# Kernel tuning notes

Hardware: AMD Instinct MI355X
Metric: run time of the kernel (lower is better)

Reference implementation:

```python
import jax, jax.numpy as jnp
import numpy as np


def setup_inputs() -> dict:
    key = jax.random.key(0)
    ks = jax.random.split(key, 5)
    B, N, Fin, Fout = 8, 2048, 512, 512
    stdv = 1.0 / np.sqrt(Fout)
    w_stdv = 1.0 / np.sqrt(Fin)
    x = jax.random.normal(ks[0], (B, N, Fin), dtype=jnp.float32)
    weight = jax.random.uniform(ks[1], (Fin, Fout), dtype=jnp.float32, minval=-stdv, maxval=stdv)
    bias = jax.random.uniform(ks[2], (Fout,), dtype=jnp.float32, minval=-stdv, maxval=stdv)
    w_one = jax.random.uniform(ks[3], (Fin, Fin), dtype=jnp.float32, minval=-w_stdv, maxval=w_stdv)
    w_two = jax.random.uniform(ks[4], (Fin, Fin), dtype=jnp.float32, minval=-w_stdv, maxval=w_stdv)
    return {"x": x, "weight": weight, "bias": bias, "w_one": w_one, "w_two": w_two}


def reference(x, weight, bias, w_one, w_two):
    # x: [B, N, Fin]
    support = jnp.einsum('bnf,fo->bno', x, weight)          # [B, N, Fout]
    phi_one = jnp.einsum('ef,bnf->ben', w_one, x)           # [B, Fin, N]
    phi_two = jnp.einsum('ef,bnf->ben', w_two, x)           # [B, Fin, N]
    adj = jnp.einsum('ben,bem->bnm', phi_one, phi_two)      # [B, N, N]
    adj = jax.nn.softmax(adj, axis=1)                        # softmax over dim=1 (columns)
    out = jnp.einsum('bnm,bmo->bno', adj, support)           # [B, N, Fout]
    return out + bias
```

## Files before the change

### kernel.cpp

```cpp
#include <hip/hip_runtime.h>
#include <math.h>

#define BB 8
#define NN 2048
#define FF 512

typedef __attribute__((ext_vector_type(8))) short short8;
typedef __attribute__((ext_vector_type(4))) float floatx4;

__device__ __forceinline__ unsigned short f2bf(float f) {
    union { float f; unsigned u; } v; v.f = f;
    unsigned r = v.u + 0x7FFFu + ((v.u >> 16) & 1u);
    return (unsigned short)(r >> 16);
}

__global__ __launch_bounds__(256) void gemm_mfma_bt(
    const unsigned short* __restrict__ A, const unsigned short* __restrict__ B,
    void* __restrict__ Cv, const float* __restrict__ bias, float* __restrict__ Dsum,
    int M, int Nc, int K, int a_ld, int b_ld, int ldc,
    long a_batch, long b_batch, long c_batch, int mode)
{
    __shared__ __align__(16) unsigned short Alds[128 * 64];
    __shared__ __align__(16) unsigned short Blds[128 * 64];

    const int tid  = threadIdx.x;
    const int wave = tid >> 6;
    const int lane = tid & 63;
    const int bz   = blockIdx.z;

    const unsigned short* Ab = A + (long)bz * a_batch;
    const unsigned short* Bb = B + (long)bz * b_batch;

    const int m0 = blockIdx.y * 128;
    const int n0 = blockIdx.x * 128;

    const int wm   = (wave >> 1) * 64;
    const int wn   = (wave & 1) * 64;
    const int fl   = lane & 15;
    const int quad = lane >> 4;

    floatx4 acc[4][4] = {};

    for (int k0 = 0; k0 < K; k0 += 64) {
        #pragma unroll
        for (int issue = 0; issue < 4; ++issue) {
            const int cbase = issue * 256 + wave * 64;
            const int c = cbase + lane;
            const int row = c >> 3;
            const int kq = ((c & 7) ^ ((c >> 3) & 7)) * 8;
            const unsigned short* gA = Ab + (long)(m0 + row) * a_ld + k0 + kq;
            __builtin_amdgcn_global_load_lds(
                (const __attribute__((address_space(1))) void*)gA,
                (__attribute__((address_space(3))) void*)&Alds[cbase * 8], 16, 0, 0);
            const unsigned short* gB = Bb + (long)(n0 + row) * b_ld + k0 + kq;
            __builtin_amdgcn_global_load_lds(
                (const __attribute__((address_space(1))) void*)gB,
                (__attribute__((address_space(3))) void*)&Blds[cbase * 8], 16, 0, 0);
        }
        __syncthreads();

        #pragma unroll
        for (int s = 0; s < 2; ++s) {
            short8 af[4], bf[4];
            #pragma unroll
            for (int i = 0; i < 4; ++i) {
                const int slot = ((s * 4 + quad) ^ (fl & 7)) * 8;
                af[i] = *(const short8*)&Alds[(wm + i * 16 + fl) * 64 + slot];
            }
            #pragma unroll
            for (int j = 0; j < 4; ++j) {
                const int slot = ((s * 4 + quad) ^ (fl & 7)) * 8;
                bf[j] = *(const short8*)&Blds[(wn + j * 16 + fl) * 64 + slot];
            }
            #pragma unroll
            for (int i = 0; i < 4; ++i)
                #pragma unroll
                for (int j = 0; j < 4; ++j)
                    acc[i][j] = __builtin_amdgcn_mfma_f32_16x16x32_bf16(af[i], bf[j], acc[i][j], 0, 0, 0);
        }
        __syncthreads();
    }

    if (mode == 0) {
        float* Cb = (float*)Cv + (long)bz * c_batch;
        #pragma unroll
        for (int j = 0; j < 4; ++j) {
            const int ng = n0 + wn + j * 16 + fl;
            const float badd = bias ? bias[ng] : 0.0f;
            #pragma unroll
            for (int i = 0; i < 4; ++i) {
                const int mg = m0 + wm + i * 16 + quad * 4;
                #pragma unroll
                for (int r = 0; r < 4; ++r)
                    Cb[(long)(mg + r) * ldc + ng] = acc[i][j][r] + badd;
            }
        }
    } else if (mode == 1) {
        unsigned short* Cb = (unsigned short*)Cv + (long)bz * c_batch;
        #pragma unroll
        for (int j = 0; j < 4; ++j) {
            const int ng = n0 + wn + j * 16 + fl;
            #pragma unroll
            for (int i = 0; i < 4; ++i) {
                const int mg = m0 + wm + i * 16 + quad * 4;
                #pragma unroll
                for (int r = 0; r < 4; ++r)
                    Cb[(long)(mg + r) * ldc + ng] = f2bf(acc[i][j][r]);
            }
        }
    } else {
        unsigned short* Cb = (unsigned short*)Cv + (long)bz * c_batch;
        float* Db = Dsum + (long)bz * NN;
        #pragma unroll
        for (int j = 0; j < 4; ++j) {
            const int ng = n0 + wn + j * 16 + fl;
            float csum = 0.f;
            #pragma unroll
            for (int i = 0; i < 4; ++i) {
                const int mg = m0 + wm + i * 16 + quad * 4;
                #pragma unroll
                for (int r = 0; r < 4; ++r) {
                    const float e = __expf(acc[i][j][r]);
                    csum += e;
                    Cb[(long)(mg + r) * ldc + ng] = f2bf(e);
                }
            }
            csum += __shfl_xor(csum, 16);
            csum += __shfl_xor(csum, 32);
            if (quad == 0) atomicAdd(&Db[ng], csum);
        }
    }
}

__global__ __launch_bounds__(256) void convert_all(
    const float* __restrict__ x, const float* __restrict__ w1, const float* __restrict__ w2,
    unsigned short* __restrict__ xb, unsigned short* __restrict__ w1b, unsigned short* __restrict__ w2b)
{
    const long NX = (long)BB * NN * FF / 8;
    const long NW = (long)FF * FF / 8;
    long t = (long)blockIdx.x * 256 + threadIdx.x;
    const float* in; unsigned short* out;
    if (t < NX) { in = x; out = xb; }
    else if (t < NX + NW) { in = w1; out = w1b; t -= NX; }
    else if (t < NX + 2 * NW) { in = w2; out = w2b; t -= NX + NW; }
    else return;
    const long i = t * 8;
    float4 a = *(const float4*)(in + i);
    float4 b = *(const float4*)(in + i + 4);
    short8 o;
    o[0] = (short)f2bf(a.x); o[1] = (short)f2bf(a.y);
    o[2] = (short)f2bf(a.z); o[3] = (short)f2bf(a.w);
    o[4] = (short)f2bf(b.x); o[5] = (short)f2bf(b.y);
    o[6] = (short)f2bf(b.z); o[7] = (short)f2bf(b.w);
    *(short8*)(out + i) = o;
}

__global__ __launch_bounds__(256) void transpose_convert(
    const float* __restrict__ in, unsigned short* __restrict__ out, int dim)
{
    __shared__ float t[32][33];
    const int tx = threadIdx.x & 31, ty = threadIdx.x >> 5;
    const int x0 = blockIdx.x * 32, y0 = blockIdx.y * 32;
    #pragma unroll
    for (int k = 0; k < 32; k += 8)
        t[ty + k][tx] = in[(long)(y0 + ty + k) * dim + x0 + tx];
    __syncthreads();
    #pragma unroll
    for (int k = 0; k < 32; k += 8)
        out[(long)(x0 + ty + k) * dim + y0 + tx] = f2bf(t[tx][ty + k]);
}

__global__ __launch_bounds__(256) void zero_f32(float* __restrict__ p, long n)
{
    long i = (long)blockIdx.x * 256 + threadIdx.x;
    if (i < n) p[i] = 0.0f;
}

__global__ __launch_bounds__(256) void scale_transpose(
    const unsigned short* __restrict__ Call, const float* __restrict__ D,
    unsigned short* __restrict__ supT, int batch0)
{
    __shared__ float t[32][33];
    __shared__ float rD[32];
    const int tx = threadIdx.x & 31, ty = threadIdx.x >> 5;
    const int mt = blockIdx.x * 32, ot = blockIdx.y * 32;
    const int b = batch0 + blockIdx.z;
    const unsigned short* Cb = Call + (long)b * NN * 1536;
    unsigned short* Tb = supT + (long)b * NN * FF;
    if (threadIdx.x < 32) rD[threadIdx.x] = 1.0f / D[(long)b * NN + mt + threadIdx.x];
    __syncthreads();
    #pragma unroll
    for (int k = 0; k < 32; k += 8) {
        unsigned short u = Cb[(long)(mt + ty + k) * 1536 + 1024 + ot + tx];
        union { unsigned uu; float f; } cv; cv.uu = ((unsigned)u) << 16;
        t[ty + k][tx] = cv.f;
    }
    __syncthreads();
    #pragma unroll
    for (int k = 0; k < 32; k += 8)
        Tb[(long)(ot + ty + k) * NN + mt + tx] = f2bf(t[tx][ty + k] * rD[tx]);
}

extern "C" void kernel_launch(void* const* d_in, const int* in_sizes, int n_in,
                              void* d_out, int out_size, void* d_ws, size_t ws_size,
                              hipStream_t stream)
{
    const float* x      = (const float*)d_in[0];
    const float* weight = (const float*)d_in[1];
    const float* bias   = (const float*)d_in[2];
    const float* w_one  = (const float*)d_in[3];
    const float* w_two  = (const float*)d_in[4];
    float* out = (float*)d_out;

    const long NF  = (long)NN * FF;
    const long NN2 = (long)NN * NN;
    const long CROW = 1536;

    char* p = (char*)d_ws;
    unsigned short* xb    = (unsigned short*)p; p += (size_t)BB * NF * 2;
    unsigned short* Wall  = (unsigned short*)p; p += (size_t)CROW * FF * 2;
    unsigned short* Call  = (unsigned short*)p; p += (size_t)BB * NN * CROW * 2;
    unsigned short* supT  = (unsigned short*)p; p += (size_t)BB * NF * 2;
    float*          Dsum  = (float*)p;          p += (size_t)BB * NN * 4;
    unsigned short* E     = (unsigned short*)p;
    unsigned short* w1b = Wall;
    unsigned short* w2b = Wall + (size_t)FF * FF;
    unsigned short* wTb = Wall + (size_t)2 * FF * FF;

    const size_t fixed = (size_t)(p - (char*)d_ws);
    const bool full = ws_size >= fixed + (size_t)BB * NN2 * 2;

    dim3 blk(256);

    convert_all<<<dim3(4352), blk, 0, stream>>>(x, w_one, w_two, xb, w1b, w2b);
    transpose_convert<<<dim3(FF / 32, FF / 32), blk, 0, stream>>>(weight, wTb, FF);
    zero_f32<<<dim3((BB * NN) / 256), blk, 0, stream>>>(Dsum, BB * NN);

    gemm_mfma_bt<<<dim3(CROW / 128, NN / 128, BB), blk, 0, stream>>>(
        xb, Wall, Call, nullptr, nullptr, NN, (int)CROW, FF,
        FF, FF, (int)CROW, NF, 0, NN * CROW, 1);

    if (full) {
        gemm_mfma_bt<<<dim3(NN / 128, NN / 128, BB), blk, 0, stream>>>(
            Call, Call + FF, E, nullptr, Dsum, NN, NN, FF,
            (int)CROW, (int)CROW, NN, NN * CROW, NN * CROW, NN2, 2);
        scale_transpose<<<dim3(NN / 32, FF / 32, BB), blk, 0, stream>>>(Call, Dsum, supT, 0);
        gemm_mfma_bt<<<dim3(FF / 128, NN / 128, BB), blk, 0, stream>>>(
            E, supT, out, bias, nullptr, NN, FF, NN,
            NN, NN, FF, NN2, NF, NF, 0);
    } else {
        for (int b = 0; b < BB; ++b) {
            const unsigned short* Cb = Call + (size_t)b * NN * CROW;
            gemm_mfma_bt<<<dim3(NN / 128, NN / 128, 1), blk, 0, stream>>>(
                Cb, Cb + FF, E, nullptr, Dsum + (size_t)b * NN, NN, NN, FF,
                (int)CROW, (int)CROW, NN, 0, 0, 0, 2);
            scale_transpose<<<dim3(NN / 32, FF / 32, 1), blk, 0, stream>>>(Call, Dsum, supT, b);
            gemm_mfma_bt<<<dim3(FF / 128, NN / 128, 1), blk, 0, stream>>>(
                E, supT + (size_t)b * NF, out + (size_t)b * NF, bias, nullptr, NN, FF, NN,
                NN, NN, FF, 0, 0, 0, 0);
        }
    }
}
```

Baseline: 240.7 us.

## Fold log2e into w_one, use exp2, packed bf16 converts, hoist GEMM addressing

Scales w_one by log2(e) during the bf16 conversion so the softmax epilogue can call a native exp2 in place of __expf. Replaces the software bf16 rounding with packed hardware conversions in the epilogues and the convert kernel. Hoists the per-thread global-load offsets out of the K loop and advances the base pointers instead. Pre-scaling before bf16 rounding slightly changes the rounding of w_one, and the epilogue stores are still scalar 16-bit writes.

```diff
diff --git a/kernel.cpp b/kernel.cpp
--- a/kernel.cpp
+++ b/kernel.cpp
@@ -4,14 +4,33 @@
 #define BB 8
 #define NN 2048
 #define FF 512
+#define LOG2E 1.4426950408889634f
 
 typedef __attribute__((ext_vector_type(8))) short short8;
 typedef __attribute__((ext_vector_type(4))) float floatx4;
+typedef __attribute__((ext_vector_type(2))) float float2v;
+typedef __attribute__((ext_vector_type(2))) __bf16 bf16x2;
 
 __device__ __forceinline__ unsigned short f2bf(float f) {
     union { float f; unsigned u; } v; v.f = f;
     unsigned r = v.u + 0x7FFFu + ((v.u >> 16) & 1u);
     return (unsigned short)(r >> 16);
+}
+
+__device__ __forceinline__ float fexp2(float x) {
+#if __has_builtin(__builtin_amdgcn_exp2f)
+    return __builtin_amdgcn_exp2f(x);
+#else
+    return __expf(x * 0.69314718056f);
+#endif
+}
+
+__device__ __forceinline__ void pk_store(unsigned short* p0, unsigned short* p1,
+                                         float a, float b) {
+    union { bf16x2 h; unsigned short s[2]; } u;
+    float2v v; v.x = a; v.y = b;
+    u.h = __builtin_convertvector(v, bf16x2);
+    *p0 = u.s[0]; *p1 = u.s[1];
 }
 
 __global__ __launch_bounds__(256) void gemm_mfma_bt(
@@ -28,50 +47,54 @@
     const int lane = tid & 63;
     const int bz   = blockIdx.z;
 
-    const unsigned short* Ab = A + (long)bz * a_batch;
-    const unsigned short* Bb = B + (long)bz * b_batch;
-
     const int m0 = blockIdx.y * 128;
     const int n0 = blockIdx.x * 128;
+
+    const unsigned short* Aptr = A + (long)bz * a_batch + (long)m0 * a_ld;
+    const unsigned short* Bptr = B + (long)bz * b_batch + (long)n0 * b_ld;
 
     const int wm   = (wave >> 1) * 64;
     const int wn   = (wave & 1) * 64;
     const int fl   = lane & 15;
     const int quad = lane >> 4;
 
+    int offA[4], offB[4], cb[4];
+    #pragma unroll
+    for (int issue = 0; issue < 4; ++issue) {
+        const int cbase = issue * 256 + wave * 64;
+        const int c = cbase + lane;
+        const int row = c >> 3;
+        const int kq = ((c & 7) ^ ((c >> 3) & 7)) * 8;
+        offA[issue] = row * a_ld + kq;
+        offB[issue] = row * b_ld + kq;
+        cb[issue] = cbase * 8;
+    }
+
     floatx4 acc[4][4] = {};
 
     for (int k0 = 0; k0 < K; k0 += 64) {
         #pragma unroll
         for (int issue = 0; issue < 4; ++issue) {
-            const int cbase = issue * 256 + wave * 64;
-            const int c = cbase + lane;
-            const int row = c >> 3;
-            const int kq = ((c & 7) ^ ((c >> 3) & 7)) * 8;
-            const unsigned short* gA = Ab + (long)(m0 + row) * a_ld + k0 + kq;
             __builtin_amdgcn_global_load_lds(
-                (const __attribute__((address_space(1))) void*)gA,
-                (__attribute__((address_space(3))) void*)&Alds[cbase * 8], 16, 0, 0);
-            const unsigned short* gB = Bb + (long)(n0 + row) * b_ld + k0 + kq;
+                (const __attribute__((address_space(1))) void*)(Aptr + offA[issue]),
+                (__attribute__((address_space(3))) void*)&Alds[cb[issue]], 16, 0, 0);
             __builtin_amdgcn_global_load_lds(
-                (const __attribute__((address_space(1))) void*)gB,
-                (__attribute__((address_space(3))) void*)&Blds[cbase * 8], 16, 0, 0);
-        }
+                (const __attribute__((address_space(1))) void*)(Bptr + offB[issue]),
+                (__attribute__((address_space(3))) void*)&Blds[cb[issue]], 16, 0, 0);
+        }
+        Aptr += 64; Bptr += 64;
         __syncthreads();
 
         #pragma unroll
         for (int s = 0; s < 2; ++s) {
             short8 af[4], bf[4];
-            #pragma unroll
-            for (int i = 0; i < 4; ++i) {
-                const int slot = ((s * 4 + quad) ^ (fl & 7)) * 8;
+            const int slot = ((s * 4 + quad) ^ (fl & 7)) * 8;
+            #pragma unroll
+            for (int i = 0; i < 4; ++i)
                 af[i] = *(const short8*)&Alds[(wm + i * 16 + fl) * 64 + slot];
-            }
-            #pragma unroll
-            for (int j = 0; j < 4; ++j) {
-                const int slot = ((s * 4 + quad) ^ (fl & 7)) * 8;
+            #pragma unroll
+            for (int j = 0; j < 4; ++j)
                 bf[j] = *(const short8*)&Blds[(wn + j * 16 + fl) * 64 + slot];
-            }
             #pragma unroll
             for (int i = 0; i < 4; ++i)
                 #pragma unroll
@@ -103,27 +126,34 @@
             #pragma unroll
             for (int i = 0; i < 4; ++i) {
                 const int mg = m0 + wm + i * 16 + quad * 4;
-                #pragma unroll
-                for (int r = 0; r < 4; ++r)
-                    Cb[(long)(mg + r) * ldc + ng] = f2bf(acc[i][j][r]);
+                pk_store(&Cb[(long)(mg + 0) * ldc + ng], &Cb[(long)(mg + 1) * ldc + ng],
+                         acc[i][j][0], acc[i][j][1]);
+                pk_store(&Cb[(long)(mg + 2) * ldc + ng], &Cb[(long)(mg + 3) * ldc + ng],
+                         acc[i][j][2], acc[i][j][3]);
             }
         }
     } else {
         unsigned short* Cb = (unsigned short*)Cv + (long)bz * c_batch;
         float* Db = Dsum + (long)bz * NN;
         #pragma unroll
+        for (int i = 0; i < 4; ++i)
+            #pragma unroll
+            for (int j = 0; j < 4; ++j)
+                #pragma unroll
+                for (int r = 0; r < 4; ++r)
+                    acc[i][j][r] = fexp2(acc[i][j][r]);
+        #pragma unroll
         for (int j = 0; j < 4; ++j) {
             const int ng = n0 + wn + j * 16 + fl;
             float csum = 0.f;
             #pragma unroll
             for (int i = 0; i < 4; ++i) {
                 const int mg = m0 + wm + i * 16 + quad * 4;
-                #pragma unroll
-                for (int r = 0; r < 4; ++r) {
-                    const float e = __expf(acc[i][j][r]);
-                    csum += e;
-                    Cb[(long)(mg + r) * ldc + ng] = f2bf(e);
-                }
+                csum += acc[i][j][0] + acc[i][j][1] + acc[i][j][2] + acc[i][j][3];
+                pk_store(&Cb[(long)(mg + 0) * ldc + ng], &Cb[(long)(mg + 1) * ldc + ng],
+                         acc[i][j][0], acc[i][j][1]);
+                pk_store(&Cb[(long)(mg + 2) * ldc + ng], &Cb[(long)(mg + 3) * ldc + ng],
+                         acc[i][j][2], acc[i][j][3]);
             }
             csum += __shfl_xor(csum, 16);
             csum += __shfl_xor(csum, 32);
@@ -139,20 +169,21 @@
     const long NX = (long)BB * NN * FF / 8;
     const long NW = (long)FF * FF / 8;
     long t = (long)blockIdx.x * 256 + threadIdx.x;
-    const float* in; unsigned short* out;
+    const float* in; unsigned short* out; float sc = 1.0f;
     if (t < NX) { in = x; out = xb; }
-    else if (t < NX + NW) { in = w1; out = w1b; t -= NX; }
+    else if (t < NX + NW) { in = w1; out = w1b; t -= NX; sc = LOG2E; }
     else if (t < NX + 2 * NW) { in = w2; out = w2b; t -= NX + NW; }
     else return;
     const long i = t * 8;
     float4 a = *(const float4*)(in + i);
     float4 b = *(const float4*)(in + i + 4);
-    short8 o;
-    o[0] = (short)f2bf(a.x); o[1] = (short)f2bf(a.y);
-    o[2] = (short)f2bf(a.z); o[3] = (short)f2bf(a.w);
-    o[4] = (short)f2bf(b.x); o[5] = (short)f2bf(b.y);
-    o[6] = (short)f2bf(b.z); o[7] = (short)f2bf(b.w);
-    *(short8*)(out + i) = o;
+    union { bf16x2 h[4]; short8 s8; } u;
+    float2v v;
+    v.x = a.x * sc; v.y = a.y * sc; u.h[0] = __builtin_convertvector(v, bf16x2);
+    v.x = a.z * sc; v.y = a.w * sc; u.h[1] = __builtin_convertvector(v, bf16x2);
+    v.x = b.x * sc; v.y = b.y * sc; u.h[2] = __builtin_convertvector(v, bf16x2);
+    v.x = b.z * sc; v.y = b.w * sc; u.h[3] = __builtin_convertvector(v, bf16x2);
+    *(short8*)(out + i) = u.s8;
 }
 
 __global__ __launch_bounds__(256) void transpose_convert(
```

Result: no change. 240.6 us (-0.0%).
